# Performance work log

Measured on AMD Instinct MI355X. Metric: run time of the kernel, lower is better.

## Reference

```python
import jax, jax.numpy as jnp
import numpy as np

B, T, N, U = 64, 128, 128, 128  # batch, seq_len, n_features, lstm units


def setup_inputs() -> dict:
    key = jax.random.key(0)
    ks = jax.random.split(key, 8)
    s = 0.05
    return {
        "x": jax.random.normal(ks[0], (B, T, N), dtype=jnp.float32),
        "hidden_state": jnp.zeros((B, U), jnp.float32),
        "cell_state": jnp.zeros((B, U), jnp.float32),
        "lstm_kernel": jax.random.normal(ks[1], (N, 4 * U), jnp.float32) * s,
        "lstm_bias": jnp.zeros((4 * U,), jnp.float32),
        "w1_kernel": jax.random.normal(ks[2], (1, T), jnp.float32) * s,
        "w1_bias": jnp.zeros((T,), jnp.float32),
        "w2_kernel": jax.random.normal(ks[3], (2 * U, T), jnp.float32) * s,
        "w2_bias": jnp.zeros((T,), jnp.float32),
        "v_kernel": jax.random.normal(ks[4], (T, 1), jnp.float32) * s,
        "v_bias": jnp.zeros((1,), jnp.float32),
        "n": N,
    }


def reference(x, hidden_state, cell_state, lstm_kernel, lstm_bias,
              w1_kernel, w1_bias, w2_kernel, w2_bias, v_kernel, v_bias, n):
    # NewLSTM ignores the provided initial state, so every timestep's LSTM
    # runs a length-1 sequence from zero (h, c). No recurrence -> vectorize
    # over time. Keras gate order: i, f, c(g), o; recurrent kernel * 0 drops out.
    z = x @ lstm_kernel + lstm_bias                       # (B,T,4U)
    i, f, g, o = jnp.split(z, 4, axis=-1)
    c = jax.nn.sigmoid(i) * jnp.tanh(g)                   # f-gate * c_prev(=0) vanishes
    h = jax.nn.sigmoid(o) * jnp.tanh(c)                   # (B,T,U)

    # Input attention per timestep, vectorized over T.
    query = jnp.concatenate([h, c], axis=-1)              # (B,T,2U)
    s2 = query @ w2_kernel + w2_bias                      # (B,T,T)
    # w1 is Dense(T) on a size-1 feature axis: x_scalar * w1_kernel[0] + b.
    s1 = x[..., None] * w1_kernel[0] + w1_bias            # (B,T,N,T)
    score = jnp.tanh(s1 + s2[:, :, None, :])              # (B,T,N,T)
    e = jnp.einsum('btnk,k->btn', score, v_kernel[:, 0]) + v_bias[0]  # (B,T,N)
    alpha = jax.nn.softmax(e, axis=-1)                    # softmax over features

    return x * alpha                                      # (B,T,N)
```

## Files before the change

### kernel.cpp

```cpp
#include <hip/hip_runtime.h>
#include <math.h>


typedef __attribute__((ext_vector_type(8))) short short8;
typedef __attribute__((ext_vector_type(4))) float f32x4;

#define BT 8192
#define NF 128
#define XP 132
#define NNODE 12
#define NSPAN 9.f
#define K_C     2.8853900817779268f
#define K_LOG2E 1.4426950408889634f

__device__ __forceinline__ float fast_rcp(float x)  { return __builtin_amdgcn_rcpf(x); }
__device__ __forceinline__ float fast_exp2(float x) { return __builtin_amdgcn_exp2f(x); }

__device__ __forceinline__ float tanh_nc(float tC) {
    return fmaf(-2.f, fast_rcp(1.f + fast_exp2(tC)), 1.f);
}
__device__ __forceinline__ float tanh_fast(float t) { return tanh_nc(t * K_C); }
__device__ __forceinline__ float sig_fast(float z) {
    return fast_rcp(1.f + fast_exp2(-K_LOG2E * z));
}
__device__ __forceinline__ unsigned short f2bf(float f) {
    unsigned u = __float_as_uint(f);
    return (unsigned short)((u + 0x7fffu + ((u >> 16) & 1u)) >> 16);
}

__global__ __launch_bounds__(64) void prep(const float* __restrict__ Wl,
                                           const float* __restrict__ w2,
                                           unsigned short* __restrict__ wsB) {
    const int lane = threadIdx.x;
    const int n16 = lane & 15, q = lane >> 4;
    const int b = blockIdx.x;
    if (b < 96) {
        const int nt = b >> 2, kk = b & 3;
        const int g = nt >> 3, jt = nt & 7;
        const int goff = (g == 0) ? 0 : (g == 1 ? 256 : 384);
        const int col = goff + jt * 16 + n16;
        unsigned short* d = wsB + b * 512 + lane * 8;
        #pragma unroll
        for (int j = 0; j < 8; j++)
            d[j] = f2bf(Wl[(kk * 32 + q * 8 + j) * 512 + col]);
    } else {
        const int fs = b - 96;
        const int nt2 = fs >> 3, kk2 = fs & 7;
        const int col = nt2 * 16 + n16;
        unsigned short* d = wsB + 49152 + fs * 512 + lane * 8;
        #pragma unroll
        for (int j = 0; j < 8; j++)
            d[j] = f2bf(w2[(kk2 * 32 + q * 8 + j) * 128 + col]);
    }
}

__global__ __launch_bounds__(512, 2) void enc(
    const float* __restrict__ x,  const unsigned short* __restrict__ wsB,
    const float* __restrict__ bl, const float* __restrict__ b2,
    const float* __restrict__ b1, const float* __restrict__ w1,
    const float* __restrict__ v,  float* __restrict__ out)
{
    __shared__ __align__(16) float xs[32][XP];
    __shared__ unsigned short Qf[2][4096];
    __shared__ __align__(16) float c2[32][XP];
    __shared__ __align__(16) float w1Cs[NF], vs[NF];
    __shared__ float Ftab[32][NNODE + 1];
    __shared__ float rowMn[32], rowMx[32];

    const int t    = threadIdx.x;
    const int lane = t & 63, w = t >> 6;
    const int n16  = lane & 15, q = lane >> 4;
    const int rowbase = blockIdx.x * 32;

    const short8* B1g = (const short8*)wsB;
    short8 b1f[3][4];
    #pragma unroll
    for (int g = 0; g < 3; g++)
        #pragma unroll
        for (int kk = 0; kk < 4; kk++)
            b1f[g][kk] = B1g[((g * 8 + w) * 4 + kk) * 64 + lane];

    #pragma unroll
    for (int p = 0; p < 2; p++) {
        const int i   = t + p * 512;
        const int row = i >> 5, col = (i & 31) * 4;
        const float4 a = *(const float4*)(x + (rowbase + row) * NF + col);
        *(float4*)&xs[row][col] = a;
        float mn = fminf(fminf(a.x, a.y), fminf(a.z, a.w));
        float mx = fmaxf(fmaxf(a.x, a.y), fmaxf(a.z, a.w));
        #pragma unroll
        for (int off = 1; off < 32; off <<= 1) {
            mn = fminf(mn, __shfl_xor(mn, off, 32));
            mx = fmaxf(mx, __shfl_xor(mx, off, 32));
        }
        if ((t & 31) == 0) { rowMn[row] = mn; rowMx[row] = mx; }
    }
    if (t < NF) { w1Cs[t] = w1[t] * K_C; vs[t] = v[t]; }
    __syncthreads();

    short8 af[2][4];
    #pragma unroll
    for (int c = 0; c < 2; c++)
        #pragma unroll
        for (int kk = 0; kk < 4; kk++) {
            const float4 v0 = *(const float4*)&xs[c * 16 + n16][kk * 32 + q * 8];
            const float4 v1 = *(const float4*)&xs[c * 16 + n16][kk * 32 + q * 8 + 4];
            short8 a;
            a[0] = f2bf(v0.x); a[1] = f2bf(v0.y); a[2] = f2bf(v0.z); a[3] = f2bf(v0.w);
            a[4] = f2bf(v1.x); a[5] = f2bf(v1.y); a[6] = f2bf(v1.z); a[7] = f2bf(v1.w);
            af[c][kk] = a;
        }

    f32x4 acc[2][3];
    #pragma unroll
    for (int c = 0; c < 2; c++)
        #pragma unroll
        for (int g = 0; g < 3; g++) acc[c][g] = (f32x4)(0.f);
    #pragma unroll
    for (int kk = 0; kk < 4; kk++)
        #pragma unroll
        for (int c = 0; c < 2; c++)
            #pragma unroll
            for (int g = 0; g < 3; g++)
                acc[c][g] = __builtin_amdgcn_mfma_f32_16x16x32_bf16(
                    af[c][kk], b1f[g][kk], acc[c][g], 0, 0, 0);

    const int u = w * 16 + n16;
    {
        const float bi = bl[u], bg = bl[256 + u], bo = bl[384 + u];
        const int kqh = u, kqc = NF + u;
        const int baseh = (kqh >> 5) * 512 + ((kqh & 31) >> 3) * 128 + q * 32 + (kqh & 7);
        const int basec = (kqc >> 5) * 512 + ((kqc & 31) >> 3) * 128 + q * 32 + (kqc & 7);
        #pragma unroll
        for (int c = 0; c < 2; c++)
            #pragma unroll
            for (int r = 0; r < 4; r++) {
                const float cc = sig_fast(acc[c][0][r] + bi) * tanh_fast(acc[c][1][r] + bg);
                const float hh = sig_fast(acc[c][2][r] + bo) * tanh_fast(cc);
                Qf[c][baseh + r * 8] = f2bf(hh);
                Qf[c][basec + r * 8] = f2bf(cc);
            }
    }
    __syncthreads();

    {
        const short8* B2g = (const short8*)(wsB + 49152);
        short8 b2f[8];
        #pragma unroll
        for (int kk2 = 0; kk2 < 8; kk2++)
            b2f[kk2] = B2g[(w * 8 + kk2) * 64 + lane];
        const float bias2 = (b2[u] + b1[u]) * K_C;
        #pragma unroll
        for (int c = 0; c < 2; c++) {
            short8 a2[8];
            #pragma unroll
            for (int kk2 = 0; kk2 < 8; kk2++)
                a2[kk2] = *(const short8*)&Qf[c][kk2 * 512 + lane * 8];
            f32x4 acc2 = (f32x4)(0.f);
            #pragma unroll
            for (int kk2 = 0; kk2 < 8; kk2++)
                acc2 = __builtin_amdgcn_mfma_f32_16x16x32_bf16(a2[kk2], b2f[kk2], acc2, 0, 0, 0);
            #pragma unroll
            for (int r = 0; r < 4; r++)
                c2[c * 16 + q * 4 + r][u] = fmaf(acc2[r], K_C, bias2);
        }
    }
    __syncthreads();

    {
        const int row = t >> 4;
        const int ks  = t & 15;
        const int k0  = ks * 8;
        const float mn = rowMn[row];
        const float h  = (rowMx[row] - mn) * (1.f / NSPAN);
        const float xi0 = mn - h;
        const float4 wa = *(const float4*)&w1Cs[k0];
        const float4 wb = *(const float4*)&w1Cs[k0 + 4];
        const float4 ca = *(const float4*)&c2[row][k0];
        const float4 cb = *(const float4*)&c2[row][k0 + 4];
        const float4 va = *(const float4*)&vs[k0];
        const float4 vb = *(const float4*)&vs[k0 + 4];
        float aC[8] = {wa.x, wa.y, wa.z, wa.w, wb.x, wb.y, wb.z, wb.w};
        float cC[8] = {ca.x, ca.y, ca.z, ca.w, cb.x, cb.y, cb.z, cb.w};
        float vv[8] = {va.x, va.y, va.z, va.w, vb.x, vb.y, vb.z, vb.w};
        float E[8], D[8], sv = 0.f;
        #pragma unroll
        for (int j = 0; j < 8; j++) {
            E[j] = fast_exp2(fmaf(aC[j], xi0, cC[j]));
            D[j] = fast_exp2(aC[j] * h);
            sv  += vv[j];
        }
        float G[NNODE];
        #pragma unroll
        for (int m = 0; m < NNODE; m++) {
            float g = 0.f;
            #pragma unroll
            for (int j = 0; j < 8; j++) {
                g = fmaf(vv[j], fast_rcp(1.f + E[j]), g);
                E[j] *= D[j];
            }
            G[m] = g;
        }
        #pragma unroll
        for (int off = 1; off < 16; off <<= 1) {
            sv += __shfl_xor(sv, off, 16);
            #pragma unroll
            for (int m = 0; m < NNODE; m++) G[m] += __shfl_xor(G[m], off, 16);
        }
        #pragma unroll
        for (int m = 0; m < NNODE; m++)
            if (ks == m) Ftab[row][m] = fmaf(-2.f, G[m], sv);
    }
    __syncthreads();

    {
        const int row = t >> 4;
        const int n0  = (t & 15) * 8;
        const float mn   = rowMn[row];
        const float span = rowMx[row] - mn;
        const float invh = span > 1e-12f ? NSPAN / span : 0.f;
        float xv[8], e8[8];
        *(float4*)&xv[0] = *(const float4*)&xs[row][n0];
        *(float4*)&xv[4] = *(const float4*)&xs[row][n0 + 4];
        #pragma unroll
        for (int i = 0; i < 8; i++) {
            const float sN = fmaf(xv[i] - mn, invh, 1.0f);
            int ii = (int)sN;
            ii = ii < 1 ? 1 : (ii > NNODE - 3 ? NNODE - 3 : ii);
            const float f  = sN - (float)ii;
            const float F0 = Ftab[row][ii - 1], F1 = Ftab[row][ii];
            const float F2 = Ftab[row][ii + 1], F3 = Ftab[row][ii + 2];
            e8[i] = F1 + 0.5f * f * ((F2 - F0)
                  + f * ((2.f * F0 - 5.f * F1 + 4.f * F2 - F3)
                  + f * (3.f * (F1 - F2) + F3 - F0)));
        }
        float mval = e8[0];
        #pragma unroll
        for (int i = 1; i < 8; i++) mval = fmaxf(mval, e8[i]);
        #pragma unroll
        for (int off = 1; off < 16; off <<= 1)
            mval = fmaxf(mval, __shfl_xor(mval, off, 16));
        float ssum = 0.f;
        #pragma unroll
        for (int i = 0; i < 8; i++) {
            e8[i] = fast_exp2(K_LOG2E * (e8[i] - mval));
            ssum += e8[i];
        }
        #pragma unroll
        for (int off = 1; off < 16; off <<= 1)
            ssum += __shfl_xor(ssum, off, 16);
        const float rs = fast_rcp(ssum);
        float4 o0, o1;
        o0.x = xv[0] * e8[0] * rs; o0.y = xv[1] * e8[1] * rs;
        o0.z = xv[2] * e8[2] * rs; o0.w = xv[3] * e8[3] * rs;
        o1.x = xv[4] * e8[4] * rs; o1.y = xv[5] * e8[5] * rs;
        o1.z = xv[6] * e8[6] * rs; o1.w = xv[7] * e8[7] * rs;
        float* op = out + (rowbase + row) * NF + n0;
        *(float4*)op       = o0;
        *(float4*)(op + 4) = o1;
    }
}

extern "C" void kernel_launch(void* const* d_in, const int* in_sizes, int n_in,
                              void* d_out, int out_size, void* d_ws, size_t ws_size,
                              hipStream_t stream) {
    const float* x  = (const float*)d_in[0];
    const float* Wl = (const float*)d_in[3];
    const float* bl = (const float*)d_in[4];
    const float* w1 = (const float*)d_in[5];
    const float* b1 = (const float*)d_in[6];
    const float* w2 = (const float*)d_in[7];
    const float* b2 = (const float*)d_in[8];
    const float* v  = (const float*)d_in[9];
    float* out = (float*)d_out;
    unsigned short* wsB = (unsigned short*)d_ws;

    prep<<<160, 64, 0, stream>>>(Wl, w2, wsB);
    enc<<<BT / 32, 512, 0, stream>>>(x, wsB, bl, b2, b1, w1, v, out);
}
```

Measured before the change: 86.56 us.

## Shrink encoder blocks to 16 rows and 128 threads, looping over unit tiles

The encoder kernel now gives each block 16 rows and 2 waves instead of 32 rows and 8 waves, which doubles the grid to 512 blocks. Each wave loops over 4 column tiles for both MFMA GEMMs and loads its B fragments from global memory per tile. The spline-table and softmax stages now use 8 threads per row with 16 elements each. The aim is better CU occupancy and load balance with smaller LDS per block, at the cost of each block re-reading the weight fragments for only 16 rows.

```diff
diff --git a/kernel.cpp b/kernel.cpp
--- a/kernel.cpp
+++ b/kernel.cpp
@@ -54,35 +54,27 @@
     }
 }
 
-__global__ __launch_bounds__(512, 2) void enc(
+__global__ __launch_bounds__(128, 3) void enc(
     const float* __restrict__ x,  const unsigned short* __restrict__ wsB,
     const float* __restrict__ bl, const float* __restrict__ b2,
     const float* __restrict__ b1, const float* __restrict__ w1,
     const float* __restrict__ v,  float* __restrict__ out)
 {
-    __shared__ __align__(16) float xs[32][XP];
-    __shared__ unsigned short Qf[2][4096];
-    __shared__ __align__(16) float c2[32][XP];
+    __shared__ __align__(16) float xs[16][XP];
+    __shared__ unsigned short Qf[4096];
+    __shared__ __align__(16) float c2[16][XP];
     __shared__ __align__(16) float w1Cs[NF], vs[NF];
-    __shared__ float Ftab[32][NNODE + 1];
-    __shared__ float rowMn[32], rowMx[32];
+    __shared__ float Ftab[16][13];
+    __shared__ float rowMn[16], rowMx[16];
 
     const int t    = threadIdx.x;
     const int lane = t & 63, w = t >> 6;
     const int n16  = lane & 15, q = lane >> 4;
-    const int rowbase = blockIdx.x * 32;
-
-    const short8* B1g = (const short8*)wsB;
-    short8 b1f[3][4];
+    const int rowbase = blockIdx.x * 16;
+
     #pragma unroll
-    for (int g = 0; g < 3; g++)
-        #pragma unroll
-        for (int kk = 0; kk < 4; kk++)
-            b1f[g][kk] = B1g[((g * 8 + w) * 4 + kk) * 64 + lane];
-
-    #pragma unroll
-    for (int p = 0; p < 2; p++) {
-        const int i   = t + p * 512;
+    for (int p = 0; p < 4; p++) {
+        const int i   = t + p * 128;
         const int row = i >> 5, col = (i & 31) * 4;
         const float4 a = *(const float4*)(x + (rowbase + row) * NF + col);
         *(float4*)&xs[row][col] = a;
@@ -95,169 +87,180 @@
         }
         if ((t & 31) == 0) { rowMn[row] = mn; rowMx[row] = mx; }
     }
-    if (t < NF) { w1Cs[t] = w1[t] * K_C; vs[t] = v[t]; }
-    __syncthreads();
-
-    short8 af[2][4];
+    w1Cs[t] = w1[t] * K_C;
+    vs[t]   = v[t];
+    __syncthreads();
+
+    short8 af[4];
     #pragma unroll
-    for (int c = 0; c < 2; c++)
-        #pragma unroll
-        for (int kk = 0; kk < 4; kk++) {
-            const float4 v0 = *(const float4*)&xs[c * 16 + n16][kk * 32 + q * 8];
-            const float4 v1 = *(const float4*)&xs[c * 16 + n16][kk * 32 + q * 8 + 4];
-            short8 a;
-            a[0] = f2bf(v0.x); a[1] = f2bf(v0.y); a[2] = f2bf(v0.z); a[3] = f2bf(v0.w);
-            a[4] = f2bf(v1.x); a[5] = f2bf(v1.y); a[6] = f2bf(v1.z); a[7] = f2bf(v1.w);
-            af[c][kk] = a;
-        }
-
-    f32x4 acc[2][3];
+    for (int kk = 0; kk < 4; kk++) {
+        const float4 v0 = *(const float4*)&xs[n16][kk * 32 + q * 8];
+        const float4 v1 = *(const float4*)&xs[n16][kk * 32 + q * 8 + 4];
+        short8 a;
+        a[0] = f2bf(v0.x); a[1] = f2bf(v0.y); a[2] = f2bf(v0.z); a[3] = f2bf(v0.w);
+        a[4] = f2bf(v1.x); a[5] = f2bf(v1.y); a[6] = f2bf(v1.z); a[7] = f2bf(v1.w);
+        af[kk] = a;
+    }
+
+    const short8* B1g = (const short8*)wsB;
     #pragma unroll
-    for (int c = 0; c < 2; c++)
-        #pragma unroll
-        for (int g = 0; g < 3; g++) acc[c][g] = (f32x4)(0.f);
-    #pragma unroll
-    for (int kk = 0; kk < 4; kk++)
-        #pragma unroll
-        for (int c = 0; c < 2; c++)
+    for (int j4 = 0; j4 < 4; j4++) {
+        const int jt = w * 4 + j4;
+        short8 bf[3][4];
+        #pragma unroll
+        for (int g = 0; g < 3; g++)
+            #pragma unroll
+            for (int kk = 0; kk < 4; kk++)
+                bf[g][kk] = B1g[((g * 8 + jt) * 4 + kk) * 64 + lane];
+        f32x4 acc[3];
+        #pragma unroll
+        for (int g = 0; g < 3; g++) acc[g] = (f32x4)(0.f);
+        #pragma unroll
+        for (int kk = 0; kk < 4; kk++)
             #pragma unroll
             for (int g = 0; g < 3; g++)
-                acc[c][g] = __builtin_amdgcn_mfma_f32_16x16x32_bf16(
-                    af[c][kk], b1f[g][kk], acc[c][g], 0, 0, 0);
-
-    const int u = w * 16 + n16;
+                acc[g] = __builtin_amdgcn_mfma_f32_16x16x32_bf16(
+                    af[kk], bf[g][kk], acc[g], 0, 0, 0);
+
+        const int u = jt * 16 + n16;
+        const float bi = bl[u], bg = bl[256 + u], bo = bl[384 + u];
+        const int kqc = NF + u;
+        const int baseh = (u >> 5) * 512 + ((u & 31) >> 3) * 128 + q * 32 + (u & 7);
+        const int basec = (kqc >> 5) * 512 + ((kqc & 31) >> 3) * 128 + q * 32 + (kqc & 7);
+        #pragma unroll
+        for (int r = 0; r < 4; r++) {
+            const float cc = sig_fast(acc[0][r] + bi) * tanh_fast(acc[1][r] + bg);
+            const float hh = sig_fast(acc[2][r] + bo) * tanh_fast(cc);
+            Qf[baseh + r * 8] = f2bf(hh);
+            Qf[basec + r * 8] = f2bf(cc);
+        }
+    }
+    __syncthreads();
+
     {
-        const float bi = bl[u], bg = bl[256 + u], bo = bl[384 + u];
-        const int kqh = u, kqc = NF + u;
-        const int baseh = (kqh >> 5) * 512 + ((kqh & 31) >> 3) * 128 + q * 32 + (kqh & 7);
-        const int basec = (kqc >> 5) * 512 + ((kqc & 31) >> 3) * 128 + q * 32 + (kqc & 7);
-        #pragma unroll
-        for (int c = 0; c < 2; c++)
-            #pragma unroll
-            for (int r = 0; r < 4; r++) {
-                const float cc = sig_fast(acc[c][0][r] + bi) * tanh_fast(acc[c][1][r] + bg);
-                const float hh = sig_fast(acc[c][2][r] + bo) * tanh_fast(cc);
-                Qf[c][baseh + r * 8] = f2bf(hh);
-                Qf[c][basec + r * 8] = f2bf(cc);
-            }
-    }
-    __syncthreads();
-
-    {
+        short8 a2[8];
+        #pragma unroll
+        for (int kk2 = 0; kk2 < 8; kk2++)
+            a2[kk2] = *(const short8*)&Qf[kk2 * 512 + lane * 8];
         const short8* B2g = (const short8*)(wsB + 49152);
-        short8 b2f[8];
-        #pragma unroll
-        for (int kk2 = 0; kk2 < 8; kk2++)
-            b2f[kk2] = B2g[(w * 8 + kk2) * 64 + lane];
-        const float bias2 = (b2[u] + b1[u]) * K_C;
-        #pragma unroll
-        for (int c = 0; c < 2; c++) {
-            short8 a2[8];
+        #pragma unroll
+        for (int j4 = 0; j4 < 4; j4++) {
+            const int nt2 = w * 4 + j4;
+            short8 b2f[8];
             #pragma unroll
             for (int kk2 = 0; kk2 < 8; kk2++)
-                a2[kk2] = *(const short8*)&Qf[c][kk2 * 512 + lane * 8];
+                b2f[kk2] = B2g[(nt2 * 8 + kk2) * 64 + lane];
             f32x4 acc2 = (f32x4)(0.f);
             #pragma unroll
             for (int kk2 = 0; kk2 < 8; kk2++)
                 acc2 = __builtin_amdgcn_mfma_f32_16x16x32_bf16(a2[kk2], b2f[kk2], acc2, 0, 0, 0);
+            const int u2 = nt2 * 16 + n16;
+            const float bias2 = (b2[u2] + b1[u2]) * K_C;
             #pragma unroll
             for (int r = 0; r < 4; r++)
-                c2[c * 16 + q * 4 + r][u] = fmaf(acc2[r], K_C, bias2);
+                c2[q * 4 + r][u2] = fmaf(acc2[r], K_C, bias2);
         }
     }
     __syncthreads();
 
     {
-        const int row = t >> 4;
-        const int ks  = t & 15;
-        const int k0  = ks * 8;
-        const float mn = rowMn[row];
-        const float h  = (rowMx[row] - mn) * (1.f / NSPAN);
+        const int row = t >> 3, ks = t & 7;
+        const float mn  = rowMn[row];
+        const float h   = (rowMx[row] - mn) * (1.f / NSPAN);
         const float xi0 = mn - h;
-        const float4 wa = *(const float4*)&w1Cs[k0];
-        const float4 wb = *(const float4*)&w1Cs[k0 + 4];
-        const float4 ca = *(const float4*)&c2[row][k0];
-        const float4 cb = *(const float4*)&c2[row][k0 + 4];
-        const float4 va = *(const float4*)&vs[k0];
-        const float4 vb = *(const float4*)&vs[k0 + 4];
-        float aC[8] = {wa.x, wa.y, wa.z, wa.w, wb.x, wb.y, wb.z, wb.w};
-        float cC[8] = {ca.x, ca.y, ca.z, ca.w, cb.x, cb.y, cb.z, cb.w};
-        float vv[8] = {va.x, va.y, va.z, va.w, vb.x, vb.y, vb.z, vb.w};
-        float E[8], D[8], sv = 0.f;
-        #pragma unroll
-        for (int j = 0; j < 8; j++) {
-            E[j] = fast_exp2(fmaf(aC[j], xi0, cC[j]));
-            D[j] = fast_exp2(aC[j] * h);
-            sv  += vv[j];
-        }
         float G[NNODE];
         #pragma unroll
-        for (int m = 0; m < NNODE; m++) {
-            float g = 0.f;
+        for (int m = 0; m < NNODE; m++) G[m] = 0.f;
+        float sv = 0.f;
+        #pragma unroll
+        for (int half = 0; half < 2; half++) {
+            const int k0 = (ks + half * 8) * 8;
+            const float4 wa = *(const float4*)&w1Cs[k0];
+            const float4 wb = *(const float4*)&w1Cs[k0 + 4];
+            const float4 ca = *(const float4*)&c2[row][k0];
+            const float4 cb = *(const float4*)&c2[row][k0 + 4];
+            const float4 va = *(const float4*)&vs[k0];
+            const float4 vb = *(const float4*)&vs[k0 + 4];
+            float aC[8] = {wa.x, wa.y, wa.z, wa.w, wb.x, wb.y, wb.z, wb.w};
+            float cC[8] = {ca.x, ca.y, ca.z, ca.w, cb.x, cb.y, cb.z, cb.w};
+            float vv[8] = {va.x, va.y, va.z, va.w, vb.x, vb.y, vb.z, vb.w};
+            float E[8], D[8];
             #pragma unroll
             for (int j = 0; j < 8; j++) {
-                g = fmaf(vv[j], fast_rcp(1.f + E[j]), g);
-                E[j] *= D[j];
+                E[j] = fast_exp2(fmaf(aC[j], xi0, cC[j]));
+                D[j] = fast_exp2(aC[j] * h);
+                sv  += vv[j];
             }
-            G[m] = g;
-        }
-        #pragma unroll
-        for (int off = 1; off < 16; off <<= 1) {
-            sv += __shfl_xor(sv, off, 16);
-            #pragma unroll
-            for (int m = 0; m < NNODE; m++) G[m] += __shfl_xor(G[m], off, 16);
-        }
-        #pragma unroll
-        for (int m = 0; m < NNODE; m++)
-            if (ks == m) Ftab[row][m] = fmaf(-2.f, G[m], sv);
+            #pragma unroll
+            for (int m = 0; m < NNODE; m++) {
+                float g = 0.f;
+                #pragma unroll
+                for (int j = 0; j < 8; j++) {
+                    g = fmaf(vv[j], fast_rcp(1.f + E[j]), g);
+                    E[j] *= D[j];
+                }
+                G[m] += g;
+            }
+        }
+        #pragma unroll
+        for (int off = 1; off < 8; off <<= 1) {
+            sv += __shfl_xor(sv, off, 8);
+            #pragma unroll
+            for (int m = 0; m < NNODE; m++) G[m] += __shfl_xor(G[m], off, 8);
+        }
+        Ftab[row][ks] = fmaf(-2.f, G[ks], sv);
+        if (ks < 4) Ftab[row][8 + ks] = fmaf(-2.f, G[8 + ks], sv);
     }
     __syncthreads();
 
     {
-        const int row = t >> 4;
-        const int n0  = (t & 15) * 8;
+        const int row = t >> 3;
+        const int n0  = (t & 7) * 16;
         const float mn   = rowMn[row];
         const float span = rowMx[row] - mn;
         const float invh = span > 1e-12f ? NSPAN / span : 0.f;
-        float xv[8], e8[8];
-        *(float4*)&xv[0] = *(const float4*)&xs[row][n0];
-        *(float4*)&xv[4] = *(const float4*)&xs[row][n0 + 4];
-        #pragma unroll
-        for (int i = 0; i < 8; i++) {
+        float xv[16], e16[16];
+        #pragma unroll
+        for (int p = 0; p < 4; p++)
+            *(float4*)&xv[p * 4] = *(const float4*)&xs[row][n0 + p * 4];
+        #pragma unroll
+        for (int i = 0; i < 16; i++) {
             const float sN = fmaf(xv[i] - mn, invh, 1.0f);
             int ii = (int)sN;
             ii = ii < 1 ? 1 : (ii > NNODE - 3 ? NNODE - 3 : ii);
             const float f  = sN - (float)ii;
             const float F0 = Ftab[row][ii - 1], F1 = Ftab[row][ii];
             const float F2 = Ftab[row][ii + 1], F3 = Ftab[row][ii + 2];
-            e8[i] = F1 + 0.5f * f * ((F2 - F0)
-                  + f * ((2.f * F0 - 5.f * F1 + 4.f * F2 - F3)
-                  + f * (3.f * (F1 - F2) + F3 - F0)));
-        }
-        float mval = e8[0];
-        #pragma unroll
-        for (int i = 1; i < 8; i++) mval = fmaxf(mval, e8[i]);
-        #pragma unroll
-        for (int off = 1; off < 16; off <<= 1)
-            mval = fmaxf(mval, __shfl_xor(mval, off, 16));
+            e16[i] = F1 + 0.5f * f * ((F2 - F0)
+                   + f * ((2.f * F0 - 5.f * F1 + 4.f * F2 - F3)
+                   + f * (3.f * (F1 - F2) + F3 - F0)));
+        }
+        float mval = e16[0];
+        #pragma unroll
+        for (int i = 1; i < 16; i++) mval = fmaxf(mval, e16[i]);
+        #pragma unroll
+        for (int off = 1; off < 8; off <<= 1)
+            mval = fmaxf(mval, __shfl_xor(mval, off, 8));
         float ssum = 0.f;
         #pragma unroll
-        for (int i = 0; i < 8; i++) {
-            e8[i] = fast_exp2(K_LOG2E * (e8[i] - mval));
-            ssum += e8[i];
-        }
-        #pragma unroll
-        for (int off = 1; off < 16; off <<= 1)
-            ssum += __shfl_xor(ssum, off, 16);
+        for (int i = 0; i < 16; i++) {
+            e16[i] = fast_exp2(K_LOG2E * (e16[i] - mval));
+            ssum += e16[i];
+        }
+        #pragma unroll
+        for (int off = 1; off < 8; off <<= 1)
+            ssum += __shfl_xor(ssum, off, 8);
         const float rs = fast_rcp(ssum);
-        float4 o0, o1;
-        o0.x = xv[0] * e8[0] * rs; o0.y = xv[1] * e8[1] * rs;
-        o0.z = xv[2] * e8[2] * rs; o0.w = xv[3] * e8[3] * rs;
-        o1.x = xv[4] * e8[4] * rs; o1.y = xv[5] * e8[5] * rs;
-        o1.z = xv[6] * e8[6] * rs; o1.w = xv[7] * e8[7] * rs;
         float* op = out + (rowbase + row) * NF + n0;
-        *(float4*)op       = o0;
-        *(float4*)(op + 4) = o1;
+        #pragma unroll
+        for (int p = 0; p < 4; p++) {
+            float4 o;
+            o.x = xv[p * 4 + 0] * e16[p * 4 + 0] * rs;
+            o.y = xv[p * 4 + 1] * e16[p * 4 + 1] * rs;
+            o.z = xv[p * 4 + 2] * e16[p * 4 + 2] * rs;
+            o.w = xv[p * 4 + 3] * e16[p * 4 + 3] * rs;
+            *(float4*)(op + p * 4) = o;
+        }
     }
 }
 
@@ -276,5 +279,5 @@
     unsigned short* wsB = (unsigned short*)d_ws;
 
     prep<<<160, 64, 0, stream>>>(Wl, w2, wsB);
-    enc<<<BT / 32, 512, 0, stream>>>(x, wsB, bl, b2, b1, w1, v, out);
-}
+    enc<<<BT / 16, 128, 0, stream>>>(x, wsB, bl, b2, b1, w1, v, out);
+}
```

New measurement: 91.22 us. 1.05x slower.
